# Kernel tuning notes

Hardware: AMD Instinct MI355X
Metric: run time of the kernel (lower is better)

Reference implementation:

```python
import jax, jax.numpy as jnp
import numpy as np

N_NODES = 524288
BLOCK = 128
NUM_BLOCKS = N_NODES // BLOCK  # 4096
MAX_KV = 64
GRAPH_WEIGHT = 0.3


def setup_inputs() -> dict:
    key = jax.random.key(0)
    k1, k2, k3, k4, k5, k6 = jax.random.split(key, 6)
    logits = jax.random.normal(k1, (N_NODES, 1), dtype=jnp.float32)
    targets = jax.random.randint(k2, (N_NODES, 1), 0, 2).astype(jnp.float32)
    sup_mask = jax.random.bernoulli(k3, 0.2, (N_NODES,))
    ignore_mask = jax.random.bernoulli(k4, 0.1, (N_NODES,))
    kv_indices = jax.random.randint(k5, (NUM_BLOCKS, MAX_KV), 0, NUM_BLOCKS, dtype=jnp.int32)
    kv_num_blocks = jax.random.randint(k6, (NUM_BLOCKS,), 1, MAX_KV + 1, dtype=jnp.int32)
    return {
        "logits": logits,
        "targets": targets,
        "sup_mask": sup_mask,
        "ignore_mask": ignore_mask,
        "kv_indices": kv_indices,
        "kv_num_blocks": kv_num_blocks,
        "block_size": BLOCK,
    }


def reference(logits, targets, sup_mask, ignore_mask, kv_indices, kv_num_blocks, block_size):
    x = logits[:, 0]
    t = targets[:, 0]

    # --- supervised BCE-with-logits, masked mean over sup_mask ---
    # BCEWithLogits(x, t) = softplus(x) - t * x
    bce = jax.nn.softplus(x) - t * x
    sup_f = sup_mask.astype(x.dtype)
    sup_cnt = sup_f.sum()
    loss_sup = jnp.where(sup_cnt > 0, (bce * sup_f).sum() / jnp.maximum(sup_cnt, 1.0), 0.0)

    # --- blockwise graph smoothness loss ---
    p = jax.nn.sigmoid(x)
    nb = x.shape[0] // block_size
    p_blk = p.reshape(nb, block_size)                         # [nb, B]
    uncertain = (~ignore_mask) & (~sup_mask)
    unc_blk = uncertain.reshape(nb, block_size)               # [nb, B]
    keep_blk = (~ignore_mask).reshape(nb, block_size)         # [nb, B]

    max_kv = kv_indices.shape[1]
    kv_valid = jnp.arange(max_kv, dtype=kv_num_blocks.dtype)[None, :] < kv_num_blocks[:, None]  # [nb, K]

    neigh_p = p_blk[kv_indices]                               # [nb, K, B] block-sparse gather
    neigh_keep = keep_blk[kv_indices] & kv_valid[:, :, None]  # [nb, K, B]
    nk_f = neigh_keep.astype(p.dtype)
    n_cnt = nk_f.sum(axis=(1, 2))                             # [nb]
    n_mean = (neigh_p * nk_f).sum(axis=(1, 2)) / jnp.maximum(n_cnt, 1.0)  # [nb]

    unc_f = unc_blk.astype(p.dtype)
    q_cnt = unc_f.sum(axis=1)                                 # [nb]
    sq = ((p_blk - n_mean[:, None]) ** 2) * unc_f             # [nb, B]
    blk_loss = sq.sum(axis=1) / jnp.maximum(q_cnt, 1.0)       # [nb]

    valid = ((q_cnt > 0) & (n_cnt > 0)).astype(p.dtype)
    count = valid.sum()
    loss_graph = (blk_loss * valid).sum() / jnp.maximum(count, 1.0)

    return loss_sup + GRAPH_WEIGHT * loss_graph
```

## Files before the change

kernel.cpp:

```cpp
#include <hip/hip_runtime.h>
#include <stdint.h>

#define N_NODES 524288
#define BLOCK 128
#define NUM_BLOCKS 4096
#define MAX_KV 64
#define GRAPH_WEIGHT 0.3f

#define WS_SUMP 0
#define WS_CNTK 4096
#define WS_QCNT 8192
#define WS_BCEP 12288
#define WS_SUPP 16384
#define WS_GNUM 20480
#define WS_GCNT 24576

__device__ __forceinline__ bool read_mask(const void* p, int i, int byteflag) {
    if (byteflag) return ((const uint8_t*)p)[i] != 0;
    return ((const int*)p)[i] != 0;
}

__device__ __forceinline__ int detect_byteflag(const void* sup, int t, int* sh_flag) {
    if (t == 0) *sh_flag = 0;
    __syncthreads();
    const unsigned int* w = (const unsigned int*)sup;
    unsigned int a = w[t] | w[t + 128];
    if (a > 1u) *sh_flag = 1;
    __syncthreads();
    return *sh_flag;
}

__global__ void __launch_bounds__(BLOCK)
k1_per_block(const float* __restrict__ logits, const float* __restrict__ targets,
             const void* __restrict__ sup, const void* __restrict__ ign,
             float* __restrict__ ws) {
    const int b = blockIdx.x, t = threadIdx.x;
    const int i = b * BLOCK + t;
    __shared__ int sh_flag;
    const int bf = detect_byteflag(sup, t, &sh_flag);
    float x  = logits[i];
    float tg = targets[i];
    bool s = read_mask(sup, i, bf);
    bool g = read_mask(ign, i, bf);
    float bce = fmaxf(x, 0.f) + log1pf(expf(-fabsf(x))) - tg * x;
    float p = 1.f / (1.f + expf(-x));
    float v0 = g ? 0.f : p;
    float v1 = g ? 0.f : 1.f;
    float v2 = (!g && !s) ? 1.f : 0.f;
    float v3 = s ? bce : 0.f;
    float v4 = s ? 1.f : 0.f;
    for (int off = 32; off > 0; off >>= 1) {
        v0 += __shfl_down(v0, off);
        v1 += __shfl_down(v1, off);
        v2 += __shfl_down(v2, off);
        v3 += __shfl_down(v3, off);
        v4 += __shfl_down(v4, off);
    }
    __shared__ float sh[2][5];
    if ((t & 63) == 0) {
        int w = t >> 6;
        sh[w][0] = v0; sh[w][1] = v1; sh[w][2] = v2; sh[w][3] = v3; sh[w][4] = v4;
    }
    __syncthreads();
    if (t == 0) {
        ws[WS_SUMP + b] = sh[0][0] + sh[1][0];
        ws[WS_CNTK + b] = sh[0][1] + sh[1][1];
        ws[WS_QCNT + b] = sh[0][2] + sh[1][2];
        ws[WS_BCEP + b] = sh[0][3] + sh[1][3];
        ws[WS_SUPP + b] = sh[0][4] + sh[1][4];
    }
}

__global__ void __launch_bounds__(BLOCK)
k2_graph(const float* __restrict__ logits,
         const void* __restrict__ sup, const void* __restrict__ ign,
         const int* __restrict__ kvi, const int* __restrict__ kvn,
         float* __restrict__ ws) {
    const int b = blockIdx.x, t = threadIdx.x;
    __shared__ int sh_flag;
    const int bf = detect_byteflag(sup, t, &sh_flag);
    __shared__ float sh_nmean, sh_ncnt;
    if (t < 64) {
        float ns = 0.f, nc = 0.f;
        int num = kvn[b];
        if (t < num) {
            int j = kvi[b * MAX_KV + t];
            ns = ws[WS_SUMP + j];
            nc = ws[WS_CNTK + j];
        }
        for (int off = 32; off > 0; off >>= 1) {
            ns += __shfl_down(ns, off);
            nc += __shfl_down(nc, off);
        }
        if (t == 0) {
            sh_ncnt  = nc;
            sh_nmean = ns / fmaxf(nc, 1.f);
        }
    }
    __syncthreads();
    const float nmean = sh_nmean;
    const float ncnt  = sh_ncnt;
    const int i = b * BLOCK + t;
    float x = logits[i];
    bool s = read_mask(sup, i, bf);
    bool g = read_mask(ign, i, bf);
    float p = 1.f / (1.f + expf(-x));
    float d = p - nmean;
    float v = (!g && !s) ? d * d : 0.f;
    for (int off = 32; off > 0; off >>= 1)
        v += __shfl_down(v, off);
    __shared__ float shv[2];
    if ((t & 63) == 0) shv[t >> 6] = v;
    __syncthreads();
    if (t == 0) {
        float vs = shv[0] + shv[1];
        float qc = ws[WS_QCNT + b];
        bool valid = (qc > 0.f) && (ncnt > 0.f);
        ws[WS_GNUM + b] = valid ? vs / fmaxf(qc, 1.f) : 0.f;
        ws[WS_GCNT + b] = valid ? 1.f : 0.f;
    }
}

__global__ void __launch_bounds__(256)
k3_final(const float* __restrict__ ws, float* __restrict__ out) {
    const int t = threadIdx.x;
    float bce = 0.f, scnt = 0.f, gnum = 0.f, gcnt = 0.f;
    for (int b = t; b < NUM_BLOCKS; b += 256) {
        bce  += ws[WS_BCEP + b];
        scnt += ws[WS_SUPP + b];
        gnum += ws[WS_GNUM + b];
        gcnt += ws[WS_GCNT + b];
    }
    for (int off = 32; off > 0; off >>= 1) {
        bce  += __shfl_down(bce, off);
        scnt += __shfl_down(scnt, off);
        gnum += __shfl_down(gnum, off);
        gcnt += __shfl_down(gcnt, off);
    }
    __shared__ float sh[4][4];
    if ((t & 63) == 0) {
        int w = t >> 6;
        sh[w][0] = bce; sh[w][1] = scnt; sh[w][2] = gnum; sh[w][3] = gcnt;
    }
    __syncthreads();
    if (t == 0) {
        float bs = sh[0][0] + sh[1][0] + sh[2][0] + sh[3][0];
        float sc = sh[0][1] + sh[1][1] + sh[2][1] + sh[3][1];
        float gn = sh[0][2] + sh[1][2] + sh[2][2] + sh[3][2];
        float gc = sh[0][3] + sh[1][3] + sh[2][3] + sh[3][3];
        float loss_sup = (sc > 0.f) ? bs / fmaxf(sc, 1.f) : 0.f;
        float loss_graph = gn / fmaxf(gc, 1.f);
        out[0] = loss_sup + GRAPH_WEIGHT * loss_graph;
    }
}

extern "C" void kernel_launch(void* const* d_in, const int* in_sizes, int n_in,
                              void* d_out, int out_size, void* d_ws, size_t ws_size,
                              hipStream_t stream) {
    const float* logits  = (const float*)d_in[0];
    const float* targets = (const float*)d_in[1];
    const void*  sup     = d_in[2];
    const void*  ign     = d_in[3];
    const int*   kvi     = (const int*)d_in[4];
    const int*   kvn     = (const int*)d_in[5];
    float* out = (float*)d_out;
    float* ws  = (float*)d_ws;

    k1_per_block<<<NUM_BLOCKS, BLOCK, 0, stream>>>(logits, targets, sup, ign, ws);
    k2_graph<<<NUM_BLOCKS, BLOCK, 0, stream>>>(logits, sup, ign, kvi, kvn, ws);
    k3_final<<<1, 256, 0, stream>>>(ws, out);
}
```

Before: 82.12 us.

## Fuse three kernels into one cooperative kernel with grid-wide syncs

Replaces the three-kernel sequence with a single cooperative kernel of 512 blocks of 256 threads. Each block handles eight node blocks and uses vectorized float4 and int4 loads in the first phase. Grid syncs separate the per-block reduction, the neighbor gather, and the final reduction, which removes two kernel launch gaps. The old kernels stay as a fallback if the cooperative launch fails. The cost is grid-sync overhead and the limits that cooperative launch places on occupancy.

Result: slower. 242.7 us (+195.6%).

```diff
diff --git a/kernel.cpp b/kernel.cpp
--- a/kernel.cpp
+++ b/kernel.cpp
@@ -1,11 +1,17 @@
 #include <hip/hip_runtime.h>
+#include <hip/hip_cooperative_groups.h>
 #include <stdint.h>
+
+namespace cg = cooperative_groups;
 
 #define N_NODES 524288
 #define BLOCK 128
 #define NUM_BLOCKS 4096
 #define MAX_KV 64
 #define GRAPH_WEIGHT 0.3f
+
+#define GRID_BLOCKS 512
+#define THREADS 256
 
 #define WS_SUMP 0
 #define WS_CNTK 4096
@@ -15,19 +21,154 @@
 #define WS_GNUM 20480
 #define WS_GCNT 24576
 
-__device__ __forceinline__ bool read_mask(const void* p, int i, int byteflag) {
-    if (byteflag) return ((const uint8_t*)p)[i] != 0;
-    return ((const int*)p)[i] != 0;
+__device__ __forceinline__ float sigmoidf_(float x) { return 1.f / (1.f + expf(-x)); }
+__device__ __forceinline__ float bcef_(float x, float tg) {
+    return fmaxf(x, 0.f) + log1pf(expf(-fabsf(x))) - tg * x;
 }
 
 __device__ __forceinline__ int detect_byteflag(const void* sup, int t, int* sh_flag) {
     if (t == 0) *sh_flag = 0;
     __syncthreads();
-    const unsigned int* w = (const unsigned int*)sup;
-    unsigned int a = w[t] | w[t + 128];
+    unsigned int a = ((const unsigned int*)sup)[t & 255];
     if (a > 1u) *sh_flag = 1;
     __syncthreads();
     return *sh_flag;
+}
+
+__global__ void __launch_bounds__(THREADS)
+fused_coop(const float* __restrict__ logits, const float* __restrict__ targets,
+           const void* __restrict__ sup, const void* __restrict__ ign,
+           const int* __restrict__ kvi, const int* __restrict__ kvn,
+           float* __restrict__ ws, float* __restrict__ out) {
+    cg::grid_group grid = cg::this_grid();
+    const int t = threadIdx.x;
+    const int wave = t >> 6, lane = t & 63;
+    __shared__ int sh_flag;
+    const int bf = detect_byteflag(sup, t, &sh_flag);
+
+    {
+        const int sub = t >> 5;
+        const int nb  = (blockIdx.x << 3) + sub;
+        const int l32 = t & 31;
+        const int base = (nb << 7) + (l32 << 2);
+        const float4 x4  = *(const float4*)(logits  + base);
+        const float4 tg4 = *(const float4*)(targets + base);
+        bool s[4], g[4];
+        if (bf) {
+            unsigned sw = *(const unsigned*)((const uint8_t*)sup + base);
+            unsigned gw = *(const unsigned*)((const uint8_t*)ign + base);
+            #pragma unroll
+            for (int k = 0; k < 4; ++k) {
+                s[k] = ((sw >> (8 * k)) & 0xffu) != 0;
+                g[k] = ((gw >> (8 * k)) & 0xffu) != 0;
+            }
+        } else {
+            int4 sv = *(const int4*)((const int*)sup + base);
+            int4 gv = *(const int4*)((const int*)ign + base);
+            s[0] = sv.x; s[1] = sv.y; s[2] = sv.z; s[3] = sv.w;
+            g[0] = gv.x; g[1] = gv.y; g[2] = gv.z; g[3] = gv.w;
+        }
+        const float x[4]  = {x4.x, x4.y, x4.z, x4.w};
+        const float tg[4] = {tg4.x, tg4.y, tg4.z, tg4.w};
+        float v0 = 0.f, v1 = 0.f, v2 = 0.f, v3 = 0.f, v4 = 0.f;
+        #pragma unroll
+        for (int k = 0; k < 4; ++k) {
+            float p = sigmoidf_(x[k]);
+            if (!g[k]) { v0 += p; v1 += 1.f; if (!s[k]) v2 += 1.f; }
+            if (s[k])  { v3 += bcef_(x[k], tg[k]); v4 += 1.f; }
+        }
+        #pragma unroll
+        for (int off = 16; off > 0; off >>= 1) {
+            v0 += __shfl_down(v0, off, 32);
+            v1 += __shfl_down(v1, off, 32);
+            v2 += __shfl_down(v2, off, 32);
+            v3 += __shfl_down(v3, off, 32);
+            v4 += __shfl_down(v4, off, 32);
+        }
+        if (l32 == 0) {
+            ws[WS_SUMP + nb] = v0;
+            ws[WS_CNTK + nb] = v1;
+            ws[WS_QCNT + nb] = v2;
+            ws[WS_BCEP + nb] = v3;
+            ws[WS_SUPP + nb] = v4;
+        }
+    }
+    __threadfence();
+    grid.sync();
+
+    #pragma unroll
+    for (int pass = 0; pass < 2; ++pass) {
+        const int nb = (blockIdx.x << 3) + (pass << 2) + wave;
+        const int num = kvn[nb];
+        float ns = 0.f, nc = 0.f;
+        if (lane < num) {
+            int j = kvi[(nb << 6) + lane];
+            ns = ws[WS_SUMP + j];
+            nc = ws[WS_CNTK + j];
+        }
+        #pragma unroll
+        for (int off = 32; off > 0; off >>= 1) {
+            ns += __shfl_down(ns, off);
+            nc += __shfl_down(nc, off);
+        }
+        ns = __shfl(ns, 0); nc = __shfl(nc, 0);
+        const float nmean = ns / fmaxf(nc, 1.f);
+        const int base = (nb << 7) + (lane << 1);
+        const float2 x2 = *(const float2*)(logits + base);
+        bool s0, s1, g0, g1;
+        if (bf) {
+            const uint8_t* sb = (const uint8_t*)sup;
+            const uint8_t* gb = (const uint8_t*)ign;
+            s0 = sb[base]; s1 = sb[base + 1];
+            g0 = gb[base]; g1 = gb[base + 1];
+        } else {
+            const int* si = (const int*)sup;
+            const int* gi = (const int*)ign;
+            s0 = si[base]; s1 = si[base + 1];
+            g0 = gi[base]; g1 = gi[base + 1];
+        }
+        float d0 = sigmoidf_(x2.x) - nmean;
+        float d1 = sigmoidf_(x2.y) - nmean;
+        float v = ((!g0 && !s0) ? d0 * d0 : 0.f) + ((!g1 && !s1) ? d1 * d1 : 0.f);
+        #pragma unroll
+        for (int off = 32; off > 0; off >>= 1) v += __shfl_down(v, off);
+        if (lane == 0) {
+            float qc = ws[WS_QCNT + nb];
+            bool valid = (qc > 0.f) && (nc > 0.f);
+            ws[WS_GNUM + nb] = valid ? v / fmaxf(qc, 1.f) : 0.f;
+            ws[WS_GCNT + nb] = valid ? 1.f : 0.f;
+        }
+    }
+    __threadfence();
+    grid.sync();
+
+    if (blockIdx.x == 0) {
+        float bce = 0.f, scnt = 0.f, gnum = 0.f, gcnt = 0.f;
+        for (int b = t; b < NUM_BLOCKS; b += THREADS) {
+            bce  += ws[WS_BCEP + b];
+            scnt += ws[WS_SUPP + b];
+            gnum += ws[WS_GNUM + b];
+            gcnt += ws[WS_GCNT + b];
+        }
+        #pragma unroll
+        for (int off = 32; off > 0; off >>= 1) {
+            bce  += __shfl_down(bce, off);
+            scnt += __shfl_down(scnt, off);
+            gnum += __shfl_down(gnum, off);
+            gcnt += __shfl_down(gcnt, off);
+        }
+        __shared__ float sh[4][4];
+        if (lane == 0) { sh[wave][0] = bce; sh[wave][1] = scnt; sh[wave][2] = gnum; sh[wave][3] = gcnt; }
+        __syncthreads();
+        if (t == 0) {
+            float bs = sh[0][0] + sh[1][0] + sh[2][0] + sh[3][0];
+            float sc = sh[0][1] + sh[1][1] + sh[2][1] + sh[3][1];
+            float gn = sh[0][2] + sh[1][2] + sh[2][2] + sh[3][2];
+            float gc = sh[0][3] + sh[1][3] + sh[2][3] + sh[3][3];
+            float loss_sup = (sc > 0.f) ? bs / fmaxf(sc, 1.f) : 0.f;
+            out[0] = loss_sup + GRAPH_WEIGHT * (gn / fmaxf(gc, 1.f));
+        }
+    }
 }
 
 __global__ void __launch_bounds__(BLOCK)
@@ -38,29 +179,19 @@
     const int i = b * BLOCK + t;
     __shared__ int sh_flag;
     const int bf = detect_byteflag(sup, t, &sh_flag);
-    float x  = logits[i];
-    float tg = targets[i];
-    bool s = read_mask(sup, i, bf);
-    bool g = read_mask(ign, i, bf);
-    float bce = fmaxf(x, 0.f) + log1pf(expf(-fabsf(x))) - tg * x;
-    float p = 1.f / (1.f + expf(-x));
-    float v0 = g ? 0.f : p;
-    float v1 = g ? 0.f : 1.f;
-    float v2 = (!g && !s) ? 1.f : 0.f;
-    float v3 = s ? bce : 0.f;
-    float v4 = s ? 1.f : 0.f;
+    float x = logits[i], tg = targets[i];
+    bool s = bf ? (((const uint8_t*)sup)[i] != 0) : (((const int*)sup)[i] != 0);
+    bool g = bf ? (((const uint8_t*)ign)[i] != 0) : (((const int*)ign)[i] != 0);
+    float bce = bcef_(x, tg);
+    float p = sigmoidf_(x);
+    float v0 = g ? 0.f : p, v1 = g ? 0.f : 1.f, v2 = (!g && !s) ? 1.f : 0.f;
+    float v3 = s ? bce : 0.f, v4 = s ? 1.f : 0.f;
     for (int off = 32; off > 0; off >>= 1) {
-        v0 += __shfl_down(v0, off);
-        v1 += __shfl_down(v1, off);
-        v2 += __shfl_down(v2, off);
-        v3 += __shfl_down(v3, off);
-        v4 += __shfl_down(v4, off);
+        v0 += __shfl_down(v0, off); v1 += __shfl_down(v1, off); v2 += __shfl_down(v2, off);
+        v3 += __shfl_down(v3, off); v4 += __shfl_down(v4, off);
     }
     __shared__ float sh[2][5];
-    if ((t & 63) == 0) {
-        int w = t >> 6;
-        sh[w][0] = v0; sh[w][1] = v1; sh[w][2] = v2; sh[w][3] = v3; sh[w][4] = v4;
-    }
+    if ((t & 63) == 0) { int w = t >> 6; sh[w][0]=v0; sh[w][1]=v1; sh[w][2]=v2; sh[w][3]=v3; sh[w][4]=v4; }
     __syncthreads();
     if (t == 0) {
         ws[WS_SUMP + b] = sh[0][0] + sh[1][0];
@@ -83,32 +214,19 @@
     if (t < 64) {
         float ns = 0.f, nc = 0.f;
         int num = kvn[b];
-        if (t < num) {
-            int j = kvi[b * MAX_KV + t];
-            ns = ws[WS_SUMP + j];
-            nc = ws[WS_CNTK + j];
-        }
-        for (int off = 32; off > 0; off >>= 1) {
-            ns += __shfl_down(ns, off);
-            nc += __shfl_down(nc, off);
-        }
-        if (t == 0) {
-            sh_ncnt  = nc;
-            sh_nmean = ns / fmaxf(nc, 1.f);
-        }
-    }
-    __syncthreads();
-    const float nmean = sh_nmean;
-    const float ncnt  = sh_ncnt;
+        if (t < num) { int j = kvi[b * MAX_KV + t]; ns = ws[WS_SUMP + j]; nc = ws[WS_CNTK + j]; }
+        for (int off = 32; off > 0; off >>= 1) { ns += __shfl_down(ns, off); nc += __shfl_down(nc, off); }
+        if (t == 0) { sh_ncnt = nc; sh_nmean = ns / fmaxf(nc, 1.f); }
+    }
+    __syncthreads();
+    const float nmean = sh_nmean, ncnt = sh_ncnt;
     const int i = b * BLOCK + t;
     float x = logits[i];
-    bool s = read_mask(sup, i, bf);
-    bool g = read_mask(ign, i, bf);
-    float p = 1.f / (1.f + expf(-x));
-    float d = p - nmean;
+    bool s = bf ? (((const uint8_t*)sup)[i] != 0) : (((const int*)sup)[i] != 0);
+    bool g = bf ? (((const uint8_t*)ign)[i] != 0) : (((const int*)ign)[i] != 0);
+    float d = sigmoidf_(x) - nmean;
     float v = (!g && !s) ? d * d : 0.f;
-    for (int off = 32; off > 0; off >>= 1)
-        v += __shfl_down(v, off);
+    for (int off = 32; off > 0; off >>= 1) v += __shfl_down(v, off);
     __shared__ float shv[2];
     if ((t & 63) == 0) shv[t >> 6] = v;
     __syncthreads();
@@ -126,31 +244,23 @@
     const int t = threadIdx.x;
     float bce = 0.f, scnt = 0.f, gnum = 0.f, gcnt = 0.f;
     for (int b = t; b < NUM_BLOCKS; b += 256) {
-        bce  += ws[WS_BCEP + b];
-        scnt += ws[WS_SUPP + b];
-        gnum += ws[WS_GNUM + b];
-        gcnt += ws[WS_GCNT + b];
+        bce += ws[WS_BCEP + b]; scnt += ws[WS_SUPP + b];
+        gnum += ws[WS_GNUM + b]; gcnt += ws[WS_GCNT + b];
     }
     for (int off = 32; off > 0; off >>= 1) {
-        bce  += __shfl_down(bce, off);
-        scnt += __shfl_down(scnt, off);
-        gnum += __shfl_down(gnum, off);
-        gcnt += __shfl_down(gcnt, off);
+        bce += __shfl_down(bce, off); scnt += __shfl_down(scnt, off);
+        gnum += __shfl_down(gnum, off); gcnt += __shfl_down(gcnt, off);
     }
     __shared__ float sh[4][4];
-    if ((t & 63) == 0) {
-        int w = t >> 6;
-        sh[w][0] = bce; sh[w][1] = scnt; sh[w][2] = gnum; sh[w][3] = gcnt;
-    }
+    if ((t & 63) == 0) { int w = t >> 6; sh[w][0]=bce; sh[w][1]=scnt; sh[w][2]=gnum; sh[w][3]=gcnt; }
     __syncthreads();
     if (t == 0) {
-        float bs = sh[0][0] + sh[1][0] + sh[2][0] + sh[3][0];
-        float sc = sh[0][1] + sh[1][1] + sh[2][1] + sh[3][1];
-        float gn = sh[0][2] + sh[1][2] + sh[2][2] + sh[3][2];
-        float gc = sh[0][3] + sh[1][3] + sh[2][3] + sh[3][3];
+        float bs = sh[0][0]+sh[1][0]+sh[2][0]+sh[3][0];
+        float sc = sh[0][1]+sh[1][1]+sh[2][1]+sh[3][1];
+        float gn = sh[0][2]+sh[1][2]+sh[2][2]+sh[3][2];
+        float gc = sh[0][3]+sh[1][3]+sh[2][3]+sh[3][3];
         float loss_sup = (sc > 0.f) ? bs / fmaxf(sc, 1.f) : 0.f;
-        float loss_graph = gn / fmaxf(gc, 1.f);
-        out[0] = loss_sup + GRAPH_WEIGHT * loss_graph;
+        out[0] = loss_sup + GRAPH_WEIGHT * (gn / fmaxf(gc, 1.f));
     }
 }
 
@@ -166,7 +276,15 @@
     float* out = (float*)d_out;
     float* ws  = (float*)d_ws;
 
-    k1_per_block<<<NUM_BLOCKS, BLOCK, 0, stream>>>(logits, targets, sup, ign, ws);
-    k2_graph<<<NUM_BLOCKS, BLOCK, 0, stream>>>(logits, sup, ign, kvi, kvn, ws);
-    k3_final<<<1, 256, 0, stream>>>(ws, out);
-}
+    void* args[] = {(void*)&logits, (void*)&targets, (void*)&sup, (void*)&ign,
+                    (void*)&kvi, (void*)&kvn, (void*)&ws, (void*)&out};
+    hipError_t err = hipLaunchCooperativeKernel((void*)fused_coop,
+                                                dim3(GRID_BLOCKS), dim3(THREADS),
+                                                args, 0, stream);
+    if (err != hipSuccess) {
+        (void)hipGetLastError();
+        k1_per_block<<<NUM_BLOCKS, BLOCK, 0, stream>>>(logits, targets, sup, ign, ws);
+        k2_graph<<<NUM_BLOCKS, BLOCK, 0, stream>>>(logits, sup, ign, kvi, kvn, ws);
+        k3_final<<<1, 256, 0, stream>>>(ws, out);
+    }
+}
```
